# Kernel tuning notes

Measured on AMD Instinct MI355X. Metric: run time of the kernel, lower is better.

The kernel has to match this reference:

```python
import jax, jax.numpy as jnp
import numpy as np

E = 1024   # embed_size
H = 16     # num_heads
D = E // H # head_dim
B, S = 4, 2048

def setup_inputs() -> dict:
    key = jax.random.key(0)
    ks = jax.random.split(key, 11)
    scale = 1.0 / np.sqrt(E)
    inp = {
        "Q": jax.random.normal(ks[0], (B, S, E), jnp.float32),
        "K": jax.random.normal(ks[1], (B, S, E), jnp.float32),
        "V": jax.random.normal(ks[2], (B, S, E), jnp.float32),
        "Wq": jax.random.uniform(ks[3], (E, E), jnp.float32, -scale, scale),
        "bq": jax.random.uniform(ks[4], (E,), jnp.float32, -scale, scale),
        "Wk": jax.random.uniform(ks[5], (E, E), jnp.float32, -scale, scale),
        "bk": jax.random.uniform(ks[6], (E,), jnp.float32, -scale, scale),
        "Wv": jax.random.uniform(ks[7], (E, E), jnp.float32, -scale, scale),
        "bv": jax.random.uniform(ks[8], (E,), jnp.float32, -scale, scale),
        "Wo": jax.random.uniform(ks[9], (E, E), jnp.float32, -scale, scale),
        "bo": jax.random.uniform(ks[10], (E,), jnp.float32, -scale, scale),
    }
    return inp

def reference(Q, K, V, Wq, bq, Wk, bk, Wv, bv, Wo, bo):
    b, sq, _ = Q.shape
    sk = K.shape[1]
    # Linear projections (torch Linear: x @ W.T + b), split into heads -> (b, H, s, D)
    q = (Q @ Wq.T + bq).reshape(b, sq, H, D).transpose(0, 2, 1, 3)
    k = (K @ Wk.T + bk).reshape(b, sk, H, D).transpose(0, 2, 1, 3)
    v = (V @ Wv.T + bv).reshape(b, sk, H, D).transpose(0, 2, 1, 3)
    scores = jnp.einsum('bhqd,bhkd->bhqk', q, k) / jnp.sqrt(jnp.float32(D))
    attn = jax.nn.softmax(scores, axis=-1)
    out = jnp.einsum('bhqk,bhkd->bhqd', attn, v)  # (b, H, sq, D)
    concat = out.transpose(0, 2, 1, 3).reshape(b, sq, E)
    return concat @ Wo.T + bo
```

## Files before the change

### kernel.cpp

```cpp
#include <hip/hip_runtime.h>
#include <hip/hip_bf16.h>

typedef unsigned short u16;
typedef unsigned int u32;
typedef __bf16 bf16x8 __attribute__((ext_vector_type(8)));
typedef float f32x4 __attribute__((ext_vector_type(4)));
typedef float f32x16 __attribute__((ext_vector_type(16)));
typedef unsigned int u32x2 __attribute__((ext_vector_type(2)));

constexpr int E_ = 1024, H_ = 16, D_ = 64, B_ = 4, S_ = 2048;
constexpr int GM = B_ * S_;
constexpr int GN = E_;
constexpr int GK = E_;

__device__ __forceinline__ u16 f2bf(float f) {
  union { float f; u32 u; } v; v.f = f;
  u32 r = v.u + 0x7fffu + ((v.u >> 16) & 1u);
  return (u16)(r >> 16);
}

__device__ __forceinline__ bf16x8 ld_bf16x8(const u16* p) {
  return *reinterpret_cast<const bf16x8*>(p);
}

__device__ __forceinline__ f32x4 mfma16(bf16x8 a, bf16x8 b, f32x4 c) {
  return __builtin_amdgcn_mfma_f32_16x16x32_bf16(a, b, c, 0, 0, 0);
}
__device__ __forceinline__ f32x16 mfma32(bf16x8 a, bf16x8 b, f32x16 c) {
  return __builtin_amdgcn_mfma_f32_32x32x16_bf16(a, b, c, 0, 0, 0);
}

__device__ __forceinline__ u32 cvtpk(float lo, float hi) {
  u32 r;
  asm("v_cvt_pk_bf16_f32 %0, %1, %2" : "=v"(r) : "v"(lo), "v"(hi));
  return r;
}

__device__ __forceinline__ void pl32swap(u32& a, u32& b) {
#if __has_builtin(__builtin_amdgcn_permlane32_swap)
  u32x2 r = __builtin_amdgcn_permlane32_swap(a, b, false, false);
  a = r.x; b = r.y;
#else
  asm volatile("v_permlane32_swap_b32 %0, %1" : "+v"(a), "+v"(b));
#endif
}

__device__ __forceinline__ float fexp2(float x) {
#if __has_builtin(__builtin_amdgcn_exp2f)
  return __builtin_amdgcn_exp2f(x);
#else
  return exp2f(x);
#endif
}

#define GLOAD_LDS16(gp, lp)                                                       \
  __builtin_amdgcn_global_load_lds(                                               \
      (const __attribute__((address_space(1))) u32*)(const void*)(gp),            \
      (__attribute__((address_space(3))) u32*)(void*)(lp), 16, 0, 0)

__global__ __launch_bounds__(256) void cvt7(
    const float4* __restrict__ s0, const float4* __restrict__ s1,
    const float4* __restrict__ s2, const float4* __restrict__ s3,
    const float4* __restrict__ s4, const float4* __restrict__ s5,
    const float4* __restrict__ s6,
    ushort4* __restrict__ d0, ushort4* __restrict__ d1,
    ushort4* __restrict__ d2, ushort4* __restrict__ d3,
    ushort4* __restrict__ d4, ushort4* __restrict__ d5,
    ushort4* __restrict__ d6) {
  long i = (long)blockIdx.x * 256 + threadIdx.x;
  const float4* s; ushort4* d; long j;
  if (i < 2097152L)      { s = s0; d = d0; j = i; }
  else if (i < 4194304L) { s = s1; d = d1; j = i - 2097152L; }
  else if (i < 6291456L) { s = s2; d = d2; j = i - 4194304L; }
  else if (i < 6553600L) { s = s3; d = d3; j = i - 6291456L; }
  else if (i < 6815744L) { s = s4; d = d4; j = i - 6553600L; }
  else if (i < 7077888L) { s = s5; d = d5; j = i - 6815744L; }
  else                   { s = s6; d = d6; j = i - 7077888L; }
  float4 v = s[j];
  ushort4 o;
  o.x = f2bf(v.x); o.y = f2bf(v.y); o.z = f2bf(v.z); o.w = f2bf(v.w);
  d[j] = o;
}

template <int MODE>
__global__ __launch_bounds__(256, 2) void gemm_bt(
    const u16* __restrict__ A, const u16* __restrict__ Bw,
    const float* __restrict__ bias, void* __restrict__ Cout, float scale) {
  __shared__ u16 As[128 * 32];
  __shared__ u16 Bs[128 * 32];
  const int tid = threadIdx.x;
  const int lane = tid & 63, w = tid >> 6;
  const int lr = lane & 15, lg = lane >> 4;
  const int bid = blockIdx.x;
  const int flat = (bid & 7) * 64 + (bid >> 3);
  const int bm = flat >> 3, bn = flat & 7;
  const int wm = (w >> 1) * 64, wn = (w & 1) * 64;

  f32x4 acc[4][4] = {};

  const int byte0 = (w * 2 + 0) * 1024 + lane * 16;
  const int byte1 = (w * 2 + 1) * 1024 + lane * 16;
  const int r0 = byte0 >> 6, c0 = (byte0 & 63) >> 1;
  const int r1 = byte1 >> 6, c1 = (byte1 & 63) >> 1;
  const u16* Arow0 = A + (size_t)(bm * 128 + r0) * GK + c0;
  const u16* Arow1 = A + (size_t)(bm * 128 + r1) * GK + c1;
  const u16* Brow0 = Bw + (size_t)(bn * 128 + r0) * GK + c0;
  const u16* Brow1 = Bw + (size_t)(bn * 128 + r1) * GK + c1;
  u16* As0 = &As[(w * 2 + 0) * 512];
  u16* As1 = &As[(w * 2 + 1) * 512];
  u16* Bs0 = &Bs[(w * 2 + 0) * 512];
  u16* Bs1 = &Bs[(w * 2 + 1) * 512];

  for (int kt = 0; kt < GK / 32; ++kt) {
    const int ko = kt * 32;
    GLOAD_LDS16(Arow0 + ko, As0);
    GLOAD_LDS16(Arow1 + ko, As1);
    GLOAD_LDS16(Brow0 + ko, Bs0);
    GLOAD_LDS16(Brow1 + ko, Bs1);
    __syncthreads();
    bf16x8 af[4], bf_[4];
#pragma unroll
    for (int mi = 0; mi < 4; ++mi)
      af[mi] = ld_bf16x8(&As[(wm + mi * 16 + lr) * 32 + lg * 8]);
#pragma unroll
    for (int ni = 0; ni < 4; ++ni)
      bf_[ni] = ld_bf16x8(&Bs[(wn + ni * 16 + lr) * 32 + lg * 8]);
#pragma unroll
    for (int mi = 0; mi < 4; ++mi)
#pragma unroll
      for (int ni = 0; ni < 4; ++ni)
        acc[mi][ni] = mfma16(af[mi], bf_[ni], acc[mi][ni]);
    __syncthreads();
  }

#pragma unroll
  for (int mi = 0; mi < 4; ++mi)
#pragma unroll
    for (int ni = 0; ni < 4; ++ni) {
      const int n = bn * 128 + wn + ni * 16 + lr;
      const float bv = bias[n];
#pragma unroll
      for (int r = 0; r < 4; ++r) {
        const int m = bm * 128 + wm + mi * 16 + lg * 4 + r;
        const float vv = (acc[mi][ni][r] + bv) * scale;
        const int b = m >> 11, s = m & 2047, h = n >> 6, d = n & 63;
        if (MODE == 0) {
          ((u16*)Cout)[(((size_t)(b * 16 + h) * 2048 + s) * 64) + d] = f2bf(vv);
        } else if (MODE == 1) {
          const int bh = b * 16 + h;
          const int t = s >> 6, ks = (s >> 4) & 3, h2 = (s >> 3) & 1, j = s & 7;
          const int dt = d >> 5, lane2 = h2 * 32 + (d & 31);
          ((u16*)Cout)[(size_t)(bh * 32 + t) * 4096 + (dt * 4 + ks) * 512 +
                       lane2 * 8 + j] = f2bf(vv);
        } else if (MODE == 3) {
          const int bh = b * 16 + h;
          const int t = s >> 6, st = (s >> 5) & 1, l31k = s & 31;
          const int kc = d >> 4, h2 = (d >> 3) & 1, j = d & 7;
          ((u16*)Cout)[(size_t)(bh * 32 + t) * 4096 + (st * 4 + kc) * 512 +
                       (h2 * 32 + l31k) * 8 + j] = f2bf(vv);
        } else {
          ((float*)Cout)[(size_t)m * 1024 + n] = vv;
        }
      }
    }
}

__global__ __launch_bounds__(256, 2) void attn9(
    const u16* __restrict__ q, const u16* __restrict__ KB,
    const u16* __restrict__ VB, u16* __restrict__ concat) {
  const int tid = threadIdx.x, lane = tid & 63, w = tid >> 6;
  const int l31 = lane & 31, hi = lane >> 5;
  const int bid = blockIdx.x;
  const int flat = (bid & 7) * 64 + (bid >> 3);
  const int bh = flat >> 3, qt = flat & 7;
  const u16* qbp = q + (size_t)bh * S_ * D_;
  const int q0 = qt * 256 + w * 64;

  bf16x8 qf[2][4];
#pragma unroll
  for (int qs = 0; qs < 2; ++qs)
#pragma unroll
    for (int kc = 0; kc < 4; ++kc)
      qf[qs][kc] =
          ld_bf16x8(&qbp[(size_t)(q0 + qs * 32 + l31) * 64 + kc * 16 + hi * 8]);

  f32x16 acc[2][2] = {};
  float l_[2] = {0.f, 0.f};

  const u16* kbase = KB + (size_t)bh * S_ * D_ + lane * 8;
  const u16* vbase = VB + (size_t)bh * S_ * D_ + lane * 8;

  for (int t = 0; t < S_ / 64; ++t) {
    const u16* kb_t = kbase + (size_t)t * 4096;
    const u16* vb_t = vbase + (size_t)t * 4096;

    bf16x8 kf[2][4];
#pragma unroll
    for (int kc = 0; kc < 4; ++kc) {
      kf[0][kc] = ld_bf16x8(kb_t + (0 * 4 + kc) * 512);
      kf[1][kc] = ld_bf16x8(kb_t + (1 * 4 + kc) * 512);
    }
    bf16x8 vt[2][4];
#pragma unroll
    for (int ks = 0; ks < 4; ++ks) {
      vt[0][ks] = ld_bf16x8(vb_t + (0 * 4 + ks) * 512);
      vt[1][ks] = ld_bf16x8(vb_t + (1 * 4 + ks) * 512);
    }

    f32x16 sF[2][2] = {};
#pragma unroll
    for (int st = 0; st < 2; ++st)
#pragma unroll
      for (int kc = 0; kc < 4; ++kc) {
        sF[0][st] = mfma32(kf[st][kc], qf[0][kc], sF[0][st]);
        sF[1][st] = mfma32(kf[st][kc], qf[1][kc], sF[1][st]);
      }

#pragma unroll
    for (int qs = 0; qs < 2; ++qs) {
      float s0 = 0.f, s1 = 0.f, s2 = 0.f, s3 = 0.f;
#pragma unroll
      for (int st = 0; st < 2; ++st)
#pragma unroll
        for (int e = 0; e < 16; e += 4) {
          const float p0 = fexp2(sF[qs][st][e + 0]);
          const float p1 = fexp2(sF[qs][st][e + 1]);
          const float p2 = fexp2(sF[qs][st][e + 2]);
          const float p3 = fexp2(sF[qs][st][e + 3]);
          sF[qs][st][e + 0] = p0; sF[qs][st][e + 1] = p1;
          sF[qs][st][e + 2] = p2; sF[qs][st][e + 3] = p3;
          s0 += p0; s1 += p1; s2 += p2; s3 += p3;
        }
      l_[qs] += (s0 + s1) + (s2 + s3);

#pragma unroll
      for (int ks = 0; ks < 4; ++ks) {
        const int st = ks >> 1, b = (ks & 1) * 8;
        u32 w0 = cvtpk(sF[qs][st][b + 0], sF[qs][st][b + 1]);
        u32 w1 = cvtpk(sF[qs][st][b + 2], sF[qs][st][b + 3]);
        u32 w2 = cvtpk(sF[qs][st][b + 4], sF[qs][st][b + 5]);
        u32 w3 = cvtpk(sF[qs][st][b + 6], sF[qs][st][b + 7]);
        pl32swap(w0, w2);
        pl32swap(w1, w3);
        union { u32 u[4]; bf16x8 v; } pa;
        pa.u[0] = w0; pa.u[1] = w1; pa.u[2] = w2; pa.u[3] = w3;
        acc[qs][0] = mfma32(vt[0][ks], pa.v, acc[qs][0]);
        acc[qs][1] = mfma32(vt[1][ks], pa.v, acc[qs][1]);
      }
    }
  }

  const int b = bh >> 4, h = bh & 15;
#pragma unroll
  for (int qs = 0; qs < 2; ++qs) {
    u32 la = __builtin_bit_cast(u32, l_[qs]), lb = la;
    pl32swap(la, lb);
    const float lt =
        __builtin_bit_cast(float, la) + __builtin_bit_cast(float, lb);
    const float inv = 1.f / lt;
    const int s = q0 + qs * 32 + l31;
    u16* crow = concat + ((size_t)(b * 2048 + s)) * 1024 + h * 64;
#pragma unroll
    for (int dt = 0; dt < 2; ++dt)
#pragma unroll
      for (int g = 0; g < 4; ++g) {
        ushort4 o;
        o.x = f2bf(acc[qs][dt][g * 4 + 0] * inv);
        o.y = f2bf(acc[qs][dt][g * 4 + 1] * inv);
        o.z = f2bf(acc[qs][dt][g * 4 + 2] * inv);
        o.w = f2bf(acc[qs][dt][g * 4 + 3] * inv);
        *(ushort4*)&crow[dt * 32 + g * 8 + hi * 4] = o;
      }
  }
}

extern "C" void kernel_launch(void* const* d_in, const int* in_sizes, int n_in,
                              void* d_out, int out_size, void* d_ws,
                              size_t ws_size, hipStream_t stream) {
  const float* Qf = (const float*)d_in[0];
  const float* Kf = (const float*)d_in[1];
  const float* Vf = (const float*)d_in[2];
  const float* Wq = (const float*)d_in[3];
  const float* bq = (const float*)d_in[4];
  const float* Wk = (const float*)d_in[5];
  const float* bk = (const float*)d_in[6];
  const float* Wv = (const float*)d_in[7];
  const float* bv = (const float*)d_in[8];
  const float* Wo = (const float*)d_in[9];
  const float* bo = (const float*)d_in[10];

  char* ws = (char*)d_ws;
  u16* Xq = (u16*)(ws);
  u16* Xk = Xq + 8388608;
  u16* Xv = Xk + 8388608;
  u16* Wqb = (u16*)(ws + (size_t)3 * 16777216);
  u16* Wkb = Wqb + 1048576;
  u16* Wvb = Wkb + 1048576;
  u16* Wob = Wvb + 1048576;
  u16* qb = (u16*)(ws + (size_t)3 * 16777216 + 8388608);
  u16* KBb = qb + (size_t)GM * GN;
  u16* VBb = KBb + (size_t)GM * GN;
  u16* concat = Xq;

  cvt7<<<28672, 256, 0, stream>>>(
      (const float4*)Qf, (const float4*)Kf, (const float4*)Vf,
      (const float4*)Wq, (const float4*)Wk, (const float4*)Wv,
      (const float4*)Wo, (ushort4*)Xq, (ushort4*)Xk, (ushort4*)Xv,
      (ushort4*)Wqb, (ushort4*)Wkb, (ushort4*)Wvb, (ushort4*)Wob);

  gemm_bt<0><<<512, 256, 0, stream>>>(Xq, Wqb, bq, qb, 0.18033688011112042f);
  gemm_bt<3><<<512, 256, 0, stream>>>(Xk, Wkb, bk, KBb, 1.0f);
  gemm_bt<1><<<512, 256, 0, stream>>>(Xv, Wvb, bv, VBb, 1.0f);

  attn9<<<512, 256, 0, stream>>>(qb, KBb, VBb, concat);

  gemm_bt<2><<<512, 256, 0, stream>>>(concat, Wob, bo, (void*)d_out, 1.0f);
}
```

Before: 204.7 us.

## Halve per-wave query rows in attention to raise occupancy and block count

The attention kernel now gives each wave 32 query rows instead of 64, doubling the grid to 1024 blocks and raising launch bounds to 3 blocks per CU. This cuts accumulator and score registers so more waves can hide the latency of global K/V loads. In exchange each K/V tile loaded from global memory feeds half as many MFMAs, which doubles total K/V traffic through L2.

```diff
diff --git a/kernel.cpp b/kernel.cpp
--- a/kernel.cpp
+++ b/kernel.cpp
@@ -165,27 +165,24 @@
     }
 }
 
-__global__ __launch_bounds__(256, 2) void attn9(
+__global__ __launch_bounds__(256, 3) void attn10(
     const u16* __restrict__ q, const u16* __restrict__ KB,
     const u16* __restrict__ VB, u16* __restrict__ concat) {
   const int tid = threadIdx.x, lane = tid & 63, w = tid >> 6;
   const int l31 = lane & 31, hi = lane >> 5;
   const int bid = blockIdx.x;
-  const int flat = (bid & 7) * 64 + (bid >> 3);
-  const int bh = flat >> 3, qt = flat & 7;
+  const int flat = (bid & 7) * 128 + (bid >> 3);
+  const int bh = flat >> 4, qt = flat & 15;
   const u16* qbp = q + (size_t)bh * S_ * D_;
-  const int q0 = qt * 256 + w * 64;
-
-  bf16x8 qf[2][4];
-#pragma unroll
-  for (int qs = 0; qs < 2; ++qs)
-#pragma unroll
-    for (int kc = 0; kc < 4; ++kc)
-      qf[qs][kc] =
-          ld_bf16x8(&qbp[(size_t)(q0 + qs * 32 + l31) * 64 + kc * 16 + hi * 8]);
-
-  f32x16 acc[2][2] = {};
-  float l_[2] = {0.f, 0.f};
+  const int q0 = qt * 128 + w * 32;
+
+  bf16x8 qf[4];
+#pragma unroll
+  for (int kc = 0; kc < 4; ++kc)
+    qf[kc] = ld_bf16x8(&qbp[(size_t)(q0 + l31) * 64 + kc * 16 + hi * 8]);
+
+  f32x16 acc[2] = {};
+  float l_ = 0.f;
 
   const u16* kbase = KB + (size_t)bh * S_ * D_ + lane * 8;
   const u16* vbase = VB + (size_t)bh * S_ * D_ + lane * 8;
@@ -207,71 +204,63 @@
       vt[1][ks] = ld_bf16x8(vb_t + (1 * 4 + ks) * 512);
     }
 
-    f32x16 sF[2][2] = {};
+    f32x16 sF[2] = {};
 #pragma unroll
     for (int st = 0; st < 2; ++st)
 #pragma unroll
-      for (int kc = 0; kc < 4; ++kc) {
-        sF[0][st] = mfma32(kf[st][kc], qf[0][kc], sF[0][st]);
-        sF[1][st] = mfma32(kf[st][kc], qf[1][kc], sF[1][st]);
+      for (int kc = 0; kc < 4; ++kc)
+        sF[st] = mfma32(kf[st][kc], qf[kc], sF[st]);
+
+    float s0 = 0.f, s1 = 0.f, s2 = 0.f, s3 = 0.f;
+#pragma unroll
+    for (int st = 0; st < 2; ++st)
+#pragma unroll
+      for (int e = 0; e < 16; e += 4) {
+        const float p0 = fexp2(sF[st][e + 0]);
+        const float p1 = fexp2(sF[st][e + 1]);
+        const float p2 = fexp2(sF[st][e + 2]);
+        const float p3 = fexp2(sF[st][e + 3]);
+        sF[st][e + 0] = p0; sF[st][e + 1] = p1;
+        sF[st][e + 2] = p2; sF[st][e + 3] = p3;
+        s0 += p0; s1 += p1; s2 += p2; s3 += p3;
       }
-
-#pragma unroll
-    for (int qs = 0; qs < 2; ++qs) {
-      float s0 = 0.f, s1 = 0.f, s2 = 0.f, s3 = 0.f;
-#pragma unroll
-      for (int st = 0; st < 2; ++st)
-#pragma unroll
-        for (int e = 0; e < 16; e += 4) {
-          const float p0 = fexp2(sF[qs][st][e + 0]);
-          const float p1 = fexp2(sF[qs][st][e + 1]);
-          const float p2 = fexp2(sF[qs][st][e + 2]);
-          const float p3 = fexp2(sF[qs][st][e + 3]);
-          sF[qs][st][e + 0] = p0; sF[qs][st][e + 1] = p1;
-          sF[qs][st][e + 2] = p2; sF[qs][st][e + 3] = p3;
-          s0 += p0; s1 += p1; s2 += p2; s3 += p3;
-        }
-      l_[qs] += (s0 + s1) + (s2 + s3);
-
-#pragma unroll
-      for (int ks = 0; ks < 4; ++ks) {
-        const int st = ks >> 1, b = (ks & 1) * 8;
-        u32 w0 = cvtpk(sF[qs][st][b + 0], sF[qs][st][b + 1]);
-        u32 w1 = cvtpk(sF[qs][st][b + 2], sF[qs][st][b + 3]);
-        u32 w2 = cvtpk(sF[qs][st][b + 4], sF[qs][st][b + 5]);
-        u32 w3 = cvtpk(sF[qs][st][b + 6], sF[qs][st][b + 7]);
-        pl32swap(w0, w2);
-        pl32swap(w1, w3);
-        union { u32 u[4]; bf16x8 v; } pa;
-        pa.u[0] = w0; pa.u[1] = w1; pa.u[2] = w2; pa.u[3] = w3;
-        acc[qs][0] = mfma32(vt[0][ks], pa.v, acc[qs][0]);
-        acc[qs][1] = mfma32(vt[1][ks], pa.v, acc[qs][1]);
-      }
+    l_ += (s0 + s1) + (s2 + s3);
+
+#pragma unroll
+    for (int ks = 0; ks < 4; ++ks) {
+      const int st = ks >> 1, b = (ks & 1) * 8;
+      u32 w0 = cvtpk(sF[st][b + 0], sF[st][b + 1]);
+      u32 w1 = cvtpk(sF[st][b + 2], sF[st][b + 3]);
+      u32 w2 = cvtpk(sF[st][b + 4], sF[st][b + 5]);
+      u32 w3 = cvtpk(sF[st][b + 6], sF[st][b + 7]);
+      pl32swap(w0, w2);
+      pl32swap(w1, w3);
+      union { u32 u[4]; bf16x8 v; } pa;
+      pa.u[0] = w0; pa.u[1] = w1; pa.u[2] = w2; pa.u[3] = w3;
+      acc[0] = mfma32(vt[0][ks], pa.v, acc[0]);
+      acc[1] = mfma32(vt[1][ks], pa.v, acc[1]);
     }
   }
 
   const int b = bh >> 4, h = bh & 15;
-#pragma unroll
-  for (int qs = 0; qs < 2; ++qs) {
-    u32 la = __builtin_bit_cast(u32, l_[qs]), lb = la;
-    pl32swap(la, lb);
-    const float lt =
-        __builtin_bit_cast(float, la) + __builtin_bit_cast(float, lb);
-    const float inv = 1.f / lt;
-    const int s = q0 + qs * 32 + l31;
-    u16* crow = concat + ((size_t)(b * 2048 + s)) * 1024 + h * 64;
-#pragma unroll
-    for (int dt = 0; dt < 2; ++dt)
-#pragma unroll
-      for (int g = 0; g < 4; ++g) {
-        ushort4 o;
-        o.x = f2bf(acc[qs][dt][g * 4 + 0] * inv);
-        o.y = f2bf(acc[qs][dt][g * 4 + 1] * inv);
-        o.z = f2bf(acc[qs][dt][g * 4 + 2] * inv);
-        o.w = f2bf(acc[qs][dt][g * 4 + 3] * inv);
-        *(ushort4*)&crow[dt * 32 + g * 8 + hi * 4] = o;
-      }
-  }
+  u32 la = __builtin_bit_cast(u32, l_), lb = la;
+  pl32swap(la, lb);
+  const float lt =
+      __builtin_bit_cast(float, la) + __builtin_bit_cast(float, lb);
+  const float inv = 1.f / lt;
+  const int s = q0 + l31;
+  u16* crow = concat + ((size_t)(b * 2048 + s)) * 1024 + h * 64;
+#pragma unroll
+  for (int dt = 0; dt < 2; ++dt)
+#pragma unroll
+    for (int g = 0; g < 4; ++g) {
+      ushort4 o;
+      o.x = f2bf(acc[dt][g * 4 + 0] * inv);
+      o.y = f2bf(acc[dt][g * 4 + 1] * inv);
+      o.z = f2bf(acc[dt][g * 4 + 2] * inv);
+      o.w = f2bf(acc[dt][g * 4 + 3] * inv);
+      *(ushort4*)&crow[dt * 32 + g * 8 + hi * 4] = o;
+    }
 }
 
 extern "C" void kernel_launch(void* const* d_in, const int* in_sizes, int n_in,
@@ -312,7 +301,7 @@
   gemm_bt<3><<<512, 256, 0, stream>>>(Xk, Wkb, bk, KBb, 1.0f);
   gemm_bt<1><<<512, 256, 0, stream>>>(Xv, Wvb, bv, VBb, 1.0f);
 
-  attn9<<<512, 256, 0, stream>>>(qb, KBb, VBb, concat);
+  attn10<<<1024, 256, 0, stream>>>(qb, KBb, VBb, concat);
 
   gemm_bt<2><<<512, 256, 0, stream>>>(concat, Wob, bo, (void*)d_out, 1.0f);
 }
```

New measurement: 213.7 us. 1.04x slower.
